# Kernel tuning notes

Measured on AMD Instinct MI355X. Metric: run time of the kernel, lower is better.

Reference implementation:

```python
import jax, jax.numpy as jnp
import numpy as np

N_FEATURES = 16
NUM_INSTANCES = 8  # labels in [0, 8); with random labels all instances present
DELTA_V = 0.5
DELTA_D = 1.5
ALPHA, BETA, GAMMA = 1.0, 1.0, 0.001
B, H, W = 16, 512, 512


def setup_inputs() -> dict:
    key = jax.random.key(0)
    k1, k2 = jax.random.split(key)
    prediction = jax.random.normal(k1, (B, N_FEATURES, H, W), dtype=jnp.float32)
    target = jax.random.randint(k2, (B, H, W), 0, NUM_INSTANCES, dtype=jnp.int64)
    return {"prediction": prediction, "target": target}


def _per_image(pred, labels):
    # pred: [F, H, W] -> [HW, F]; labels: [H, W] -> [HW]
    F = pred.shape[0]
    x = pred.reshape(F, -1).T            # [HW, F]
    lab = labels.reshape(-1)             # [HW]
    K = NUM_INSTANCES

    counts = jax.ops.segment_sum(jnp.ones_like(lab, dtype=x.dtype), lab, num_segments=K)  # [K]
    counts = jnp.maximum(counts, 1.0)
    seg_sum = jax.ops.segment_sum(x, lab, num_segments=K)  # [K, F]
    mu = seg_sum / counts[:, None]                          # [K, F] cluster means

    # l_var: intra-cluster pull
    mu_g = mu[lab]                                          # gather [HW, F]
    d = jnp.linalg.norm(mu_g - x, axis=1) - DELTA_V         # [HW]
    d = jnp.maximum(d, 0.0) ** 2
    l_var = (jax.ops.segment_sum(d, lab, num_segments=K) / counts).sum() / K

    # l_dist: inter-cluster push (pairwise, off-diagonal via 1-eye mask)
    mu_diff = jnp.linalg.norm(mu[:, None, :] - mu[None, :, :], axis=-1)  # [K, K]
    hinge = 2.0 * DELTA_D * (1.0 - jnp.eye(K, dtype=x.dtype)) - mu_diff
    l_dist = (jnp.maximum(hinge, 0.0) ** 2).sum() / K / (K - 1)

    # l_reg
    l_reg = jnp.linalg.norm(mu, axis=1).sum() / K

    loss = ALPHA * l_var + BETA * l_dist + GAMMA * l_reg
    return jnp.stack([loss, l_var, l_dist, l_reg])


def reference(prediction, target):
    per = jax.vmap(_per_image)(prediction, target)  # [B, 4]
    return per.mean(axis=0)                          # [4]: loss, l_var, l_dist, l_reg
```

## Files before the change

kernel.cpp:

```cpp
#include <hip/hip_runtime.h>
#include <hip/hip_bf16.h>

constexpr int F_ = 16;
constexpr int K_ = 8;
constexpr int B_ = 16;
constexpr int HW_ = 512 * 512;
constexpr float DELTA_V = 0.5f;
constexpr float TWO_DELTA_D = 3.0f;
constexpr float GAMMA = 0.001f;

constexpr int CHUNKS = 64;
constexpr int PIX = HW_ / CHUNKS;
constexpr int SLOT = 136;

constexpr int NPART   = B_ * CHUNKS;
constexpr int OFF_PART = 0;
constexpr int OFF_MU   = OFF_PART + NPART * SLOT;
constexpr int OFF_INV  = OFF_MU + B_ * K_ * F_;
constexpr int OFF_IMG  = OFF_INV + B_ * K_;
constexpr int OFF_ACC  = OFF_IMG + B_ * 2;

__device__ inline float waveReduceSum(float v) {
#pragma unroll
  for (int off = 32; off > 0; off >>= 1)
    v += __shfl_down(v, off, 64);
  return v;
}

__global__ __launch_bounds__(256) void k1_sums(const float* __restrict__ pred,
                                               const int* __restrict__ tgt,
                                               float* __restrict__ ws) {
  float* part = ws + OFF_PART;
  const int b = blockIdx.y;
  const int chunk = blockIdx.x;
  const int lane = threadIdx.x;
  const int wy = threadIdx.y;

  float acc[4][8];
#pragma unroll
  for (int j = 0; j < 4; ++j)
#pragma unroll
    for (int k = 0; k < 8; ++k) acc[j][k] = 0.f;
  float cnt[8];
#pragma unroll
  for (int k = 0; k < 8; ++k) cnt[k] = 0.f;

  const int* tb = tgt + b * HW_ + chunk * PIX;
  const float* pb = pred + (size_t)b * F_ * HW_ + chunk * PIX;

  constexpr int ITERS = PIX / 256;
#pragma unroll 1
  for (int it = 0; it < ITERS; ++it) {
    const int p = it * 256 + lane * 4;
    const int4 lb = *reinterpret_cast<const int4*>(tb + p);
    const int labs[4] = {lb.x, lb.y, lb.z, lb.w};
    float sel[4][8];
#pragma unroll
    for (int pp = 0; pp < 4; ++pp)
#pragma unroll
      for (int k = 0; k < 8; ++k) sel[pp][k] = (labs[pp] == k) ? 1.f : 0.f;

#pragma unroll
    for (int j = 0; j < 4; ++j) {
      const int f = wy * 4 + j;
      const float4 x = *reinterpret_cast<const float4*>(pb + f * HW_ + p);
#pragma unroll
      for (int k = 0; k < 8; ++k) {
        acc[j][k] = fmaf(sel[0][k], x.x, acc[j][k]);
        acc[j][k] = fmaf(sel[1][k], x.y, acc[j][k]);
        acc[j][k] = fmaf(sel[2][k], x.z, acc[j][k]);
        acc[j][k] = fmaf(sel[3][k], x.w, acc[j][k]);
      }
    }
    if (wy == 0) {
#pragma unroll
      for (int k = 0; k < 8; ++k)
        cnt[k] += sel[0][k] + sel[1][k] + sel[2][k] + sel[3][k];
    }
  }

  float* slot = part + (size_t)(b * CHUNKS + chunk) * SLOT;
#pragma unroll
  for (int j = 0; j < 4; ++j)
#pragma unroll
    for (int k = 0; k < 8; ++k) {
      float v = waveReduceSum(acc[j][k]);
      if (lane == 0) slot[k * F_ + wy * 4 + j] = v;
    }
  if (wy == 0) {
#pragma unroll
    for (int k = 0; k < 8; ++k) {
      float v = waveReduceSum(cnt[k]);
      if (lane == 0) slot[128 + k] = v;
    }
  }
}

__global__ __launch_bounds__(256) void k2_mu(float* __restrict__ ws) {
  const float* part = ws + OFF_PART;
  float* invc = ws + OFF_IMG - B_ * K_;
  float* mu = ws + OFF_MU;
  float* img = ws + OFF_IMG;
  float* accum = ws + OFF_ACC;
  const int b = blockIdx.x, t = threadIdx.x;
  __shared__ float tot[SLOT];
  __shared__ float mu_s[8][17];
  __shared__ float inv_s[8];
  __shared__ float lreg_arr[8];

  if (b == 0 && t == 0) accum[0] = 0.f;

  if (t < SLOT) {
    float s = 0.f;
    const float* p = part + (size_t)b * CHUNKS * SLOT + t;
    for (int c = 0; c < CHUNKS; ++c) s += p[(size_t)c * SLOT];
    tot[t] = s;
  }
  __syncthreads();
  if (t < 8) {
    float c = fmaxf(tot[128 + t], 1.f);
    float iv = 1.f / c;
    inv_s[t] = iv;
    invc[b * K_ + t] = iv;
  }
  __syncthreads();
  if (t < 128) {
    int k = t >> 4, f = t & 15;
    float m = tot[t] * inv_s[k];
    mu[b * K_ * F_ + t] = m;
    mu_s[k][f] = m;
  }
  __syncthreads();
  if (t < 8) {
    float s = 0.f;
#pragma unroll
    for (int f = 0; f < 16; ++f) s = fmaf(mu_s[t][f], mu_s[t][f], s);
    lreg_arr[t] = sqrtf(s);
  }
  if (t < 64) {
    int a = t >> 3, c2 = t & 7;
    float v = 0.f;
    if (a != c2) {
      float dsq = 0.f;
#pragma unroll
      for (int f = 0; f < 16; ++f) {
        float dd = mu_s[a][f] - mu_s[c2][f];
        dsq = fmaf(dd, dd, dsq);
      }
      float h = fmaxf(TWO_DELTA_D - sqrtf(dsq), 0.f);
      v = h * h;
    }
    v = waveReduceSum(v);
    if (t == 0) img[b * 2 + 0] = v;
  }
  __syncthreads();
  if (t == 0) {
    float lr = 0.f;
#pragma unroll
    for (int k = 0; k < 8; ++k) lr += lreg_arr[k];
    img[b * 2 + 1] = lr;
  }
}

__global__ __launch_bounds__(256) void k3_lvar(const float* __restrict__ pred,
                                               const int* __restrict__ tgt,
                                               float* __restrict__ ws) {
  const float* mu = ws + OFF_MU;
  const float* inv = ws + OFF_INV;
  float* accum = ws + OFF_ACC;
  const int b = blockIdx.y, chunk = blockIdx.x;
  const int t = threadIdx.x;
  __shared__ float mu_s[8][17];
  __shared__ float inv_s[8];
  __shared__ float red[4];
  if (t < 128) mu_s[t >> 4][t & 15] = mu[b * K_ * F_ + t];
  if (t < 8) inv_s[t] = inv[b * K_ + t];
  __syncthreads();

  const int* tb = tgt + b * HW_ + chunk * PIX;
  const float* pb = pred + (size_t)b * F_ * HW_ + chunk * PIX;

  float lsum = 0.f;
  constexpr int ITERS = PIX / 1024;
#pragma unroll 1
  for (int it = ITERS - 1; it >= 0; --it) {
    const int p = it * 1024 + t * 4;
    const int4 lb = *reinterpret_cast<const int4*>(tb + p);
    const int labs[4] = {lb.x, lb.y, lb.z, lb.w};
    float d2[4] = {0.f, 0.f, 0.f, 0.f};
#pragma unroll
    for (int f = 15; f >= 0; --f) {
      const float4 x = *reinterpret_cast<const float4*>(pb + f * HW_ + p);
      float m0 = mu_s[labs[0]][f];
      float m1 = mu_s[labs[1]][f];
      float m2 = mu_s[labs[2]][f];
      float m3 = mu_s[labs[3]][f];
      float dd0 = x.x - m0; d2[0] = fmaf(dd0, dd0, d2[0]);
      float dd1 = x.y - m1; d2[1] = fmaf(dd1, dd1, d2[1]);
      float dd2 = x.z - m2; d2[2] = fmaf(dd2, dd2, d2[2]);
      float dd3 = x.w - m3; d2[3] = fmaf(dd3, dd3, d2[3]);
    }
#pragma unroll
    for (int pp = 0; pp < 4; ++pp) {
      float dist = sqrtf(d2[pp]);
      float h = fmaxf(dist - DELTA_V, 0.f);
      lsum = fmaf(h * h, inv_s[labs[pp]], lsum);
    }
  }
  float v = waveReduceSum(lsum);
  const int lane = t & 63, wid = t >> 6;
  if (lane == 0) red[wid] = v;
  __syncthreads();
  if (t == 0) atomicAdd(&accum[0], red[0] + red[1] + red[2] + red[3]);
}

__global__ void k4_final(const float* __restrict__ ws, float* __restrict__ out) {
  const float* img = ws + OFF_IMG;
  const float* accum = ws + OFF_ACC;
  float ld = 0.f, lr = 0.f;
#pragma unroll
  for (int b = 0; b < B_; ++b) {
    ld += img[b * 2 + 0];
    lr += img[b * 2 + 1];
  }
  float lv = accum[0] * (1.f / (K_ * (float)B_));
  ld *= 1.f / (K_ * (K_ - 1) * (float)B_);
  lr *= 1.f / (K_ * (float)B_);
  out[0] = lv + ld + GAMMA * lr;
  out[1] = lv;
  out[2] = ld;
  out[3] = lr;
}

extern "C" void kernel_launch(void* const* d_in, const int* in_sizes, int n_in,
                              void* d_out, int out_size, void* d_ws, size_t ws_size,
                              hipStream_t stream) {
  const float* pred = (const float*)d_in[0];
  const int* tgt = (const int*)d_in[1];
  float* out = (float*)d_out;
  float* ws = (float*)d_ws;

  hipLaunchKernelGGL(k1_sums, dim3(CHUNKS, B_), dim3(64, 4), 0, stream, pred, tgt, ws);
  hipLaunchKernelGGL(k2_mu, dim3(B_), dim3(256), 0, stream, ws);
  hipLaunchKernelGGL(k3_lvar, dim3(CHUNKS, B_), dim3(256), 0, stream, pred, tgt, ws);
  hipLaunchKernelGGL(k4_final, dim3(1), dim3(1), 0, stream, ws, out);
}
```

Before: 107.3 us.

## Fuse sums, means and l_var into one kernel with per-image spin barrier

Merges the segment-sum, mean/distance and l_var kernels into a single persistent-style launch. Blocks add their partial sums atomically, the last block per image computes the means and publishes a flag, and the other blocks spin-wait on that flag before the l_var pass. The aim is to cut launch gaps and let each block reread its chunk of prediction while it is still cache-resident. The l_var inner loop now reads means as float4 from shared memory. This relies on all 1024 blocks being co-resident, otherwise the spin-wait could deadlock, and atomic float adds make the summation order nondeterministic.

```diff
diff --git a/kernel.cpp b/kernel.cpp
--- a/kernel.cpp
+++ b/kernel.cpp
@@ -11,14 +11,15 @@
 
 constexpr int CHUNKS = 64;
 constexpr int PIX = HW_ / CHUNKS;
+constexpr int NBLK = B_ * CHUNKS;
 constexpr int SLOT = 136;
 
-constexpr int NPART   = B_ * CHUNKS;
-constexpr int OFF_PART = 0;
-constexpr int OFF_MU   = OFF_PART + NPART * SLOT;
-constexpr int OFF_INV  = OFF_MU + B_ * K_ * F_;
+constexpr int OFF_SUM  = 0;
+constexpr int OFF_MU   = OFF_SUM + B_ * SLOT;
+constexpr int OFF_INV  = OFF_MU + B_ * 128;
 constexpr int OFF_IMG  = OFF_INV + B_ * K_;
-constexpr int OFF_ACC  = OFF_IMG + B_ * 2;
+constexpr int OFF_LVAR = OFF_IMG + 2 * B_;
+constexpr int OFF_CTL  = OFF_LVAR + B_;
 
 __device__ inline float waveReduceSum(float v) {
 #pragma unroll
@@ -27,14 +28,51 @@
   return v;
 }
 
-__global__ __launch_bounds__(256) void k1_sums(const float* __restrict__ pred,
-                                               const int* __restrict__ tgt,
-                                               float* __restrict__ ws) {
-  float* part = ws + OFF_PART;
-  const int b = blockIdx.y;
-  const int chunk = blockIdx.x;
-  const int lane = threadIdx.x;
-  const int wy = threadIdx.y;
+__device__ inline float comp(const float4& v, int i) {
+  return i == 0 ? v.x : i == 1 ? v.y : i == 2 ? v.z : v.w;
+}
+
+__device__ inline float dload(const float* p) {
+  return __hip_atomic_load(p, __ATOMIC_RELAXED, __HIP_MEMORY_SCOPE_AGENT);
+}
+__device__ inline void dstore(float* p, float v) {
+  __hip_atomic_store(p, v, __ATOMIC_RELAXED, __HIP_MEMORY_SCOPE_AGENT);
+}
+
+__global__ void k0_init(float* __restrict__ ws) {
+  const int t = threadIdx.x;
+  for (int i = t; i < B_ * SLOT; i += 256) ws[OFF_SUM + i] = 0.f;
+  if (t < B_) ws[OFF_LVAR + t] = 0.f;
+  unsigned* ctl = (unsigned*)(ws + OFF_CTL);
+  if (t < 33) ctl[t] = 0u;
+}
+
+__global__ __launch_bounds__(256, 4) void fused(const float* __restrict__ pred,
+                                                const int* __restrict__ tgt,
+                                                float* __restrict__ ws,
+                                                float* __restrict__ out) {
+  const int bid = blockIdx.x;
+  const int b = bid >> 6, chunk = bid & 63;
+  const int t = threadIdx.x;
+  const int lane = t & 63, wy = t >> 6;
+
+  float* sum_img = ws + OFF_SUM + b * SLOT;
+  float* mu   = ws + OFF_MU;
+  float* invc = ws + OFF_INV;
+  float* img  = ws + OFF_IMG;
+  float* lvar = ws + OFF_LVAR;
+  unsigned* ctl  = (unsigned*)(ws + OFF_CTL);
+  unsigned* ctr  = ctl;
+  unsigned* flag = ctl + 16;
+  unsigned* done = ctl + 32;
+
+  __shared__ alignas(16) float mu_s[8][20];
+  __shared__ float inv_s[8];
+  __shared__ float red[4];
+  __shared__ int isred;
+
+  const int* tb = tgt + b * HW_ + chunk * PIX;
+  const float* pb = pred + (size_t)b * F_ * HW_ + chunk * PIX;
 
   float acc[4][8];
 #pragma unroll
@@ -45,12 +83,9 @@
 #pragma unroll
   for (int k = 0; k < 8; ++k) cnt[k] = 0.f;
 
-  const int* tb = tgt + b * HW_ + chunk * PIX;
-  const float* pb = pred + (size_t)b * F_ * HW_ + chunk * PIX;
-
-  constexpr int ITERS = PIX / 256;
+  constexpr int ITERS1 = PIX / 256;
 #pragma unroll 1
-  for (int it = 0; it < ITERS; ++it) {
+  for (int it = 0; it < ITERS1; ++it) {
     const int p = it * 256 + lane * 4;
     const int4 lb = *reinterpret_cast<const int4*>(tb + p);
     const int labs[4] = {lb.x, lb.y, lb.z, lb.w};
@@ -79,126 +114,117 @@
     }
   }
 
-  float* slot = part + (size_t)(b * CHUNKS + chunk) * SLOT;
 #pragma unroll
   for (int j = 0; j < 4; ++j)
 #pragma unroll
     for (int k = 0; k < 8; ++k) {
       float v = waveReduceSum(acc[j][k]);
-      if (lane == 0) slot[k * F_ + wy * 4 + j] = v;
+      if (lane == 0) atomicAdd(&sum_img[k * F_ + wy * 4 + j], v);
     }
   if (wy == 0) {
 #pragma unroll
     for (int k = 0; k < 8; ++k) {
       float v = waveReduceSum(cnt[k]);
-      if (lane == 0) slot[128 + k] = v;
-    }
-  }
-}
-
-__global__ __launch_bounds__(256) void k2_mu(float* __restrict__ ws) {
-  const float* part = ws + OFF_PART;
-  float* invc = ws + OFF_IMG - B_ * K_;
-  float* mu = ws + OFF_MU;
-  float* img = ws + OFF_IMG;
-  float* accum = ws + OFF_ACC;
-  const int b = blockIdx.x, t = threadIdx.x;
-  __shared__ float tot[SLOT];
-  __shared__ float mu_s[8][17];
-  __shared__ float inv_s[8];
-  __shared__ float lreg_arr[8];
-
-  if (b == 0 && t == 0) accum[0] = 0.f;
-
-  if (t < SLOT) {
-    float s = 0.f;
-    const float* p = part + (size_t)b * CHUNKS * SLOT + t;
-    for (int c = 0; c < CHUNKS; ++c) s += p[(size_t)c * SLOT];
-    tot[t] = s;
-  }
-  __syncthreads();
-  if (t < 8) {
-    float c = fmaxf(tot[128 + t], 1.f);
-    float iv = 1.f / c;
-    inv_s[t] = iv;
-    invc[b * K_ + t] = iv;
-  }
-  __syncthreads();
-  if (t < 128) {
-    int k = t >> 4, f = t & 15;
-    float m = tot[t] * inv_s[k];
-    mu[b * K_ * F_ + t] = m;
-    mu_s[k][f] = m;
-  }
-  __syncthreads();
-  if (t < 8) {
-    float s = 0.f;
-#pragma unroll
-    for (int f = 0; f < 16; ++f) s = fmaf(mu_s[t][f], mu_s[t][f], s);
-    lreg_arr[t] = sqrtf(s);
-  }
-  if (t < 64) {
-    int a = t >> 3, c2 = t & 7;
-    float v = 0.f;
-    if (a != c2) {
-      float dsq = 0.f;
-#pragma unroll
-      for (int f = 0; f < 16; ++f) {
-        float dd = mu_s[a][f] - mu_s[c2][f];
-        dsq = fmaf(dd, dd, dsq);
-      }
-      float h = fmaxf(TWO_DELTA_D - sqrtf(dsq), 0.f);
-      v = h * h;
-    }
-    v = waveReduceSum(v);
-    if (t == 0) img[b * 2 + 0] = v;
-  }
-  __syncthreads();
+      if (lane == 0) atomicAdd(&sum_img[128 + k], v);
+    }
+  }
+  __syncthreads();
+
   if (t == 0) {
-    float lr = 0.f;
-#pragma unroll
-    for (int k = 0; k < 8; ++k) lr += lreg_arr[k];
-    img[b * 2 + 1] = lr;
-  }
-}
-
-__global__ __launch_bounds__(256) void k3_lvar(const float* __restrict__ pred,
-                                               const int* __restrict__ tgt,
-                                               float* __restrict__ ws) {
-  const float* mu = ws + OFF_MU;
-  const float* inv = ws + OFF_INV;
-  float* accum = ws + OFF_ACC;
-  const int b = blockIdx.y, chunk = blockIdx.x;
-  const int t = threadIdx.x;
-  __shared__ float mu_s[8][17];
-  __shared__ float inv_s[8];
-  __shared__ float red[4];
-  if (t < 128) mu_s[t >> 4][t & 15] = mu[b * K_ * F_ + t];
-  if (t < 8) inv_s[t] = inv[b * K_ + t];
-  __syncthreads();
-
-  const int* tb = tgt + b * HW_ + chunk * PIX;
-  const float* pb = pred + (size_t)b * F_ * HW_ + chunk * PIX;
+    unsigned old = __hip_atomic_fetch_add(&ctr[b], 1u, __ATOMIC_ACQ_REL,
+                                          __HIP_MEMORY_SCOPE_AGENT);
+    isred = (old == (unsigned)(CHUNKS - 1));
+  }
+  __syncthreads();
+
+  if (isred) {
+    __shared__ float tot[SLOT];
+    __shared__ float lreg_sh[8];
+    if (t < SLOT) tot[t] = dload(&sum_img[t]);
+    __syncthreads();
+    if (t < 8) {
+      float c = fmaxf(tot[128 + t], 1.f);
+      float iv = 1.f / c;
+      inv_s[t] = iv;
+      dstore(&invc[b * K_ + t], iv);
+    }
+    __syncthreads();
+    if (t < 128) {
+      int k = t >> 4, f = t & 15;
+      float m = tot[t] * inv_s[k];
+      dstore(&mu[b * 128 + t], m);
+      mu_s[k][f] = m;
+    }
+    __syncthreads();
+    if (t < 8) {
+      float s = 0.f;
+#pragma unroll
+      for (int f = 0; f < 16; ++f) s = fmaf(mu_s[t][f], mu_s[t][f], s);
+      lreg_sh[t] = sqrtf(s);
+    }
+    if (t < 64) {
+      int a = t >> 3, c2 = t & 7;
+      float v = 0.f;
+      if (a != c2) {
+        float dsq = 0.f;
+#pragma unroll
+        for (int f = 0; f < 16; ++f) {
+          float dd = mu_s[a][f] - mu_s[c2][f];
+          dsq = fmaf(dd, dd, dsq);
+        }
+        float h = fmaxf(TWO_DELTA_D - sqrtf(dsq), 0.f);
+        v = h * h;
+      }
+      v = waveReduceSum(v);
+      if (t == 0) dstore(&img[b * 2 + 0], v);
+    }
+    __syncthreads();
+    if (t == 0) {
+      float lr = 0.f;
+#pragma unroll
+      for (int k = 0; k < 8; ++k) lr += lreg_sh[k];
+      dstore(&img[b * 2 + 1], lr);
+      __hip_atomic_store(&flag[b], 1u, __ATOMIC_RELEASE, __HIP_MEMORY_SCOPE_AGENT);
+    }
+  }
+
+  if (t == 0) {
+    while (__hip_atomic_load(&flag[b], __ATOMIC_ACQUIRE, __HIP_MEMORY_SCOPE_AGENT) == 0u)
+      __builtin_amdgcn_s_sleep(2);
+  }
+  __syncthreads();
+
+  if (t < 128) mu_s[t >> 4][t & 15] = dload(&mu[b * 128 + t]);
+  if (t < 8) inv_s[t] = dload(&invc[b * K_ + t]);
+  __syncthreads();
 
   float lsum = 0.f;
-  constexpr int ITERS = PIX / 1024;
+  constexpr int ITERS2 = PIX / 1024;
 #pragma unroll 1
-  for (int it = ITERS - 1; it >= 0; --it) {
+  for (int it = ITERS2 - 1; it >= 0; --it) {
     const int p = it * 1024 + t * 4;
     const int4 lb = *reinterpret_cast<const int4*>(tb + p);
     const int labs[4] = {lb.x, lb.y, lb.z, lb.w};
     float d2[4] = {0.f, 0.f, 0.f, 0.f};
 #pragma unroll
-    for (int f = 15; f >= 0; --f) {
-      const float4 x = *reinterpret_cast<const float4*>(pb + f * HW_ + p);
-      float m0 = mu_s[labs[0]][f];
-      float m1 = mu_s[labs[1]][f];
-      float m2 = mu_s[labs[2]][f];
-      float m3 = mu_s[labs[3]][f];
-      float dd0 = x.x - m0; d2[0] = fmaf(dd0, dd0, d2[0]);
-      float dd1 = x.y - m1; d2[1] = fmaf(dd1, dd1, d2[1]);
-      float dd2 = x.z - m2; d2[2] = fmaf(dd2, dd2, d2[2]);
-      float dd3 = x.w - m3; d2[3] = fmaf(dd3, dd3, d2[3]);
+    for (int f4 = 0; f4 < 4; ++f4) {
+      const float4 xr0 = *reinterpret_cast<const float4*>(pb + (f4 * 4 + 0) * HW_ + p);
+      const float4 xr1 = *reinterpret_cast<const float4*>(pb + (f4 * 4 + 1) * HW_ + p);
+      const float4 xr2 = *reinterpret_cast<const float4*>(pb + (f4 * 4 + 2) * HW_ + p);
+      const float4 xr3 = *reinterpret_cast<const float4*>(pb + (f4 * 4 + 3) * HW_ + p);
+#pragma unroll
+      for (int pp = 0; pp < 4; ++pp) {
+        const float4 m = *reinterpret_cast<const float4*>(&mu_s[labs[pp]][f4 * 4]);
+        float e0 = comp(xr0, pp) - m.x;
+        float e1 = comp(xr1, pp) - m.y;
+        float e2 = comp(xr2, pp) - m.z;
+        float e3 = comp(xr3, pp) - m.w;
+        float s = fmaf(e0, e0, 0.f);
+        s = fmaf(e1, e1, s);
+        s = fmaf(e2, e2, s);
+        s = fmaf(e3, e3, s);
+        d2[pp] += s;
+      }
     }
 #pragma unroll
     for (int pp = 0; pp < 4; ++pp) {
@@ -208,28 +234,30 @@
     }
   }
   float v = waveReduceSum(lsum);
-  const int lane = t & 63, wid = t >> 6;
-  if (lane == 0) red[wid] = v;
-  __syncthreads();
-  if (t == 0) atomicAdd(&accum[0], red[0] + red[1] + red[2] + red[3]);
-}
-
-__global__ void k4_final(const float* __restrict__ ws, float* __restrict__ out) {
-  const float* img = ws + OFF_IMG;
-  const float* accum = ws + OFF_ACC;
-  float ld = 0.f, lr = 0.f;
-#pragma unroll
-  for (int b = 0; b < B_; ++b) {
-    ld += img[b * 2 + 0];
-    lr += img[b * 2 + 1];
-  }
-  float lv = accum[0] * (1.f / (K_ * (float)B_));
-  ld *= 1.f / (K_ * (K_ - 1) * (float)B_);
-  lr *= 1.f / (K_ * (float)B_);
-  out[0] = lv + ld + GAMMA * lr;
-  out[1] = lv;
-  out[2] = ld;
-  out[3] = lr;
+  if (lane == 0) red[wy] = v;
+  __syncthreads();
+
+  if (t == 0) {
+    atomicAdd(&lvar[b], red[0] + red[1] + red[2] + red[3]);
+    unsigned d = __hip_atomic_fetch_add(done, 1u, __ATOMIC_ACQ_REL,
+                                        __HIP_MEMORY_SCOPE_AGENT);
+    if (d == (unsigned)(NBLK - 1)) {
+      float lv = 0.f, ld = 0.f, lr = 0.f;
+#pragma unroll
+      for (int bb = 0; bb < B_; ++bb) {
+        lv += dload(&lvar[bb]);
+        ld += dload(&img[bb * 2 + 0]);
+        lr += dload(&img[bb * 2 + 1]);
+      }
+      lv *= 1.f / (K_ * (float)B_);
+      ld *= 1.f / (K_ * (K_ - 1) * (float)B_);
+      lr *= 1.f / (K_ * (float)B_);
+      out[0] = lv + ld + GAMMA * lr;
+      out[1] = lv;
+      out[2] = ld;
+      out[3] = lr;
+    }
+  }
 }
 
 extern "C" void kernel_launch(void* const* d_in, const int* in_sizes, int n_in,
@@ -240,8 +268,6 @@
   float* out = (float*)d_out;
   float* ws = (float*)d_ws;
 
-  hipLaunchKernelGGL(k1_sums, dim3(CHUNKS, B_), dim3(64, 4), 0, stream, pred, tgt, ws);
-  hipLaunchKernelGGL(k2_mu, dim3(B_), dim3(256), 0, stream, ws);
-  hipLaunchKernelGGL(k3_lvar, dim3(CHUNKS, B_), dim3(256), 0, stream, pred, tgt, ws);
-  hipLaunchKernelGGL(k4_final, dim3(1), dim3(1), 0, stream, ws, out);
-}
+  hipLaunchKernelGGL(k0_init, dim3(1), dim3(256), 0, stream, ws);
+  hipLaunchKernelGGL(fused, dim3(NBLK), dim3(256), 0, stream, pred, tgt, ws, out);
+}
```

After: 216.4 us. +101.6%, slower.
